# Performance work log

Measured on AMD Instinct MI355X. Metric: run time of the kernel, lower is better.

The kernel has to match this reference:

```python
import jax, jax.numpy as jnp
import numpy as np

B, L, C_S, H = 1, 512, 384, 12
D = C_S // H  # head_dim = 32


def setup_inputs() -> dict:
    key = jax.random.key(0)
    ks = jax.random.split(key, 12)
    sc = 1.0 / np.sqrt(C_S)
    inp = {
        "s": jax.random.normal(ks[0], (B, L, C_S), dtype=jnp.float32),
        "z": jax.random.normal(ks[1], (B, L, L, C_S), dtype=jnp.float32),
        "mask": jax.random.randint(ks[2], (B, L), 0, 2, dtype=jnp.int32),
        # learned params
        "Wq": jax.random.normal(ks[3], (C_S, H * D), dtype=jnp.float32) * sc,
        "bq": jnp.zeros((H * D,), dtype=jnp.float32),
        "Wkv": jax.random.normal(ks[4], (C_S, 2 * H * D), dtype=jnp.float32) * sc,
        "bkv": jnp.zeros((2 * H * D,), dtype=jnp.float32),
        "Wb": jax.random.normal(ks[5], (C_S, H), dtype=jnp.float32) * sc,
        "bb": jnp.zeros((H,), dtype=jnp.float32),
        "Wg": jax.random.normal(ks[6], (C_S, H), dtype=jnp.float32) * sc,
        "bg": jnp.zeros((H,), dtype=jnp.float32),
        "Wout": jax.random.normal(ks[7], (H * D, C_S), dtype=jnp.float32) * sc,
        "bout": jnp.zeros((C_S,), dtype=jnp.float32),
    }
    return inp


def reference(s, z, Wq, bq, Wkv, bkv, Wb, bb, Wg, bg, Wout, bout, mask):
    b, l, c = s.shape
    q = (s @ Wq + bq).reshape(b, l, H, D)                 # (B,L,h,d)
    kv = (s @ Wkv + bkv).reshape(b, l, 2, H, D)
    k, v = kv[:, :, 0], kv[:, :, 1]                       # (B,L,h,d)
    logits = jnp.einsum('blhd,bmhd->bhlm', q, k) * (D ** -0.5)
    bias = jnp.transpose(z @ Wb + bb, (0, 3, 1, 2))       # (B,h,L,L)
    logits = logits + bias
    gate = jax.nn.sigmoid(jnp.transpose(z @ Wg + bg, (0, 3, 1, 2)))
    maskf = mask.astype(logits.dtype)
    mask2d = maskf[:, :, None] * maskf[:, None, :]        # (B,L,L)
    logits = jnp.where(mask2d[:, None] < 0.5, jnp.asarray(-1e9, logits.dtype), logits)
    attn = jax.nn.softmax(logits, axis=-1) * gate         # (B,h,L,L)
    o = jnp.einsum('bhlm,bmhd->blhd', attn, v).reshape(b, l, H * D)
    return o @ Wout + bout
```

## Files before the change

kernel.cpp:

```cpp
#include <hip/hip_runtime.h>
#include <math.h>


__global__ __launch_bounds__(256) void sgemm_bias(const float* __restrict__ A, int lda,
                                                  const float* __restrict__ B, int ldb,
                                                  const float* __restrict__ bias,
                                                  float* __restrict__ C, int ldc, int K)
{
    __shared__ float As[32 * 36];
    __shared__ float Bs[32 * 68];

    const int t  = threadIdx.x;
    const int m0 = blockIdx.y * 32;
    const int n0 = blockIdx.x * 64;
    const int tx = t & 15;
    const int ty = t >> 4;

    float acc[2][4];
    #pragma unroll
    for (int i = 0; i < 2; ++i)
        #pragma unroll
        for (int j = 0; j < 4; ++j) acc[i][j] = 0.f;

    for (int kc = 0; kc < K; kc += 32) {
        __syncthreads();
        {
            int r = t >> 3, c = (t & 7) * 4;
            float4 av = *(const float4*)&A[(size_t)(m0 + r) * lda + kc + c];
            As[(c + 0) * 36 + r] = av.x;
            As[(c + 1) * 36 + r] = av.y;
            As[(c + 2) * 36 + r] = av.z;
            As[(c + 3) * 36 + r] = av.w;
        }
        #pragma unroll
        for (int i = 0; i < 2; ++i) {
            int slot = i * 256 + t;
            int r = slot >> 4, c = (slot & 15) * 4;
            *(float4*)&Bs[r * 68 + c] = *(const float4*)&B[(size_t)(kc + r) * ldb + n0 + c];
        }
        __syncthreads();
        #pragma unroll 8
        for (int k = 0; k < 32; ++k) {
            float2 a = *(const float2*)&As[k * 36 + ty * 2];
            float4 b = *(const float4*)&Bs[k * 68 + tx * 4];
            acc[0][0] = fmaf(a.x, b.x, acc[0][0]);
            acc[0][1] = fmaf(a.x, b.y, acc[0][1]);
            acc[0][2] = fmaf(a.x, b.z, acc[0][2]);
            acc[0][3] = fmaf(a.x, b.w, acc[0][3]);
            acc[1][0] = fmaf(a.y, b.x, acc[1][0]);
            acc[1][1] = fmaf(a.y, b.y, acc[1][1]);
            acc[1][2] = fmaf(a.y, b.z, acc[1][2]);
            acc[1][3] = fmaf(a.y, b.w, acc[1][3]);
        }
    }

    float4 bv = *(const float4*)&bias[n0 + tx * 4];
    #pragma unroll
    for (int im = 0; im < 2; ++im) {
        float4 r;
        r.x = acc[im][0] + bv.x;
        r.y = acc[im][1] + bv.y;
        r.z = acc[im][2] + bv.z;
        r.w = acc[im][3] + bv.w;
        *(float4*)&C[(size_t)(m0 + ty * 2 + im) * ldc + n0 + tx * 4] = r;
    }
}

__global__ __launch_bounds__(256) void wcat_kernel(const float* __restrict__ Wb,
                                                   const float* __restrict__ Wg,
                                                   float* __restrict__ wcat)
{
    for (int idx = threadIdx.x; idx < 24 * 384; idx += 256) {
        int hh = idx / 384, k = idx % 384;
        wcat[idx] = (hh < 12) ? Wb[k * 12 + hh] : Wg[k * 12 + (hh - 12)];
    }
}

__global__ __launch_bounds__(256) void biasgate_kernel(const float* __restrict__ z,
                                                       const float* __restrict__ wcat,
                                                       const float* __restrict__ bb,
                                                       const float* __restrict__ bg,
                                                       float* __restrict__ bias_out,
                                                       float* __restrict__ gate_out)
{
    const int t = threadIdx.x;
    const size_t p = (size_t)blockIdx.x * 256 + t;
    const float* zp = z + p * 384;

    float acc[24];
    #pragma unroll
    for (int h = 0; h < 24; ++h) acc[h] = 0.f;

    for (int c = 0; c < 12; ++c) {
        const int kc = c * 32;
        float4 zr[8];
        #pragma unroll
        for (int i = 0; i < 8; ++i)
            zr[i] = *(const float4*)&zp[kc + i * 4];
        #pragma unroll
        for (int k4 = 0; k4 < 8; ++k4) {
            const float4 zv = zr[k4];
            const float* wp = wcat + kc + k4 * 4;
            #pragma unroll
            for (int hh = 0; hh < 24; ++hh) {
                float4 w = *(const float4*)&wp[hh * 384];
                acc[hh] = fmaf(zv.x, w.x,
                          fmaf(zv.y, w.y,
                          fmaf(zv.z, w.z,
                          fmaf(zv.w, w.w, acc[hh]))));
            }
        }
    }

    #pragma unroll
    for (int hh = 0; hh < 12; ++hh)
        bias_out[(size_t)hh * 262144 + p] = acc[hh] + bb[hh];
    #pragma unroll
    for (int hh = 0; hh < 12; ++hh) {
        float x = acc[12 + hh] + bg[hh];
        gate_out[(size_t)hh * 262144 + p] = 1.f / (1.f + expf(-x));
    }
}

__global__ __launch_bounds__(256) void attn_kernel(const float* __restrict__ q_ws,
                                                   const float* __restrict__ kv_ws,
                                                   const float* __restrict__ bias_ws,
                                                   const float* __restrict__ gate_ws,
                                                   const int* __restrict__ mask,
                                                   float* __restrict__ o_ws)
{
    __shared__ float ql[16 * 36];
    __shared__ float kl[128 * 36];
    __shared__ float att[16 * 516];
    __shared__ int   mint[16];

    const int t  = threadIdx.x;
    const int h  = blockIdx.y;
    const int i0 = blockIdx.x * 16;

    for (int idx = t; idx < 512; idx += 256) {
        int ii = idx >> 5, d = idx & 31;
        ql[ii * 36 + d] = q_ws[(size_t)(i0 + ii) * 384 + h * 32 + d];
    }
    if (t < 16) mint[t] = mask[i0 + t];

    const float inv = 0.17677669529663687f;
    const int jl = t & 127;
    const int ip = t >> 7;

    for (int jc = 0; jc < 4; ++jc) {
        const int j0 = jc * 128;
        __syncthreads();
        for (int idx = t; idx < 4096; idx += 256) {
            int jj = idx >> 5, d = idx & 31;
            kl[jj * 36 + d] = kv_ws[(size_t)(j0 + jj) * 768 + h * 32 + d];
        }
        __syncthreads();
        float4 kr[8];
        #pragma unroll
        for (int x = 0; x < 8; ++x) kr[x] = *(const float4*)&kl[jl * 36 + x * 4];
        const int mj = mask[j0 + jl];
        #pragma unroll
        for (int rr = 0; rr < 8; ++rr) {
            int ii = ip + rr * 2;
            float dot = 0.f;
            #pragma unroll
            for (int x = 0; x < 8; ++x) {
                float4 qv = *(const float4*)&ql[ii * 36 + x * 4];
                dot = fmaf(kr[x].x, qv.x, dot);
                dot = fmaf(kr[x].y, qv.y, dot);
                dot = fmaf(kr[x].z, qv.z, dot);
                dot = fmaf(kr[x].w, qv.w, dot);
            }
            float bv = bias_ws[((size_t)h << 18) + (size_t)(i0 + ii) * 512 + j0 + jl];
            float lg = fmaf(dot, inv, bv);
            att[ii * 516 + j0 + jl] = (mint[ii] != 0 && mj != 0) ? lg : -1e9f;
        }
    }
    __syncthreads();

    {
        const int rr = t >> 4, g = t & 15;
        const int base = rr * 516 + g;
        float mx = -3.0e38f;
        #pragma unroll
        for (int n = 0; n < 32; ++n) mx = fmaxf(mx, att[base + n * 16]);
        #pragma unroll
        for (int off = 8; off >= 1; off >>= 1) mx = fmaxf(mx, __shfl_xor(mx, off));
        float sum = 0.f;
        #pragma unroll
        for (int n = 0; n < 32; ++n) {
            float e = expf(att[base + n * 16] - mx);
            att[base + n * 16] = e;
            sum += e;
        }
        #pragma unroll
        for (int off = 8; off >= 1; off >>= 1) sum += __shfl_xor(sum, off);
        float isum = 1.f / sum;
        const size_t gbase = ((size_t)h << 18) + (size_t)(i0 + rr) * 512 + g;
        #pragma unroll
        for (int n = 0; n < 32; ++n) {
            float gt = gate_ws[gbase + n * 16];
            att[base + n * 16] *= isum * gt;
        }
    }
    __syncthreads();

    {
        const int d = t & 31, grp = t >> 5;
        const float* vp = kv_ws + 384 + h * 32 + d;
        float a0 = 0.f, a1 = 0.f;
        #pragma unroll 8
        for (int j = 0; j < 512; ++j) {
            float vv = vp[(size_t)j * 768];
            a0 = fmaf(att[grp * 516 + j], vv, a0);
            a1 = fmaf(att[(grp + 8) * 516 + j], vv, a1);
        }
        o_ws[(size_t)(i0 + grp) * 384 + h * 32 + d]     = a0;
        o_ws[(size_t)(i0 + grp + 8) * 384 + h * 32 + d] = a1;
    }
}

extern "C" void kernel_launch(void* const* d_in, const int* in_sizes, int n_in,
                              void* d_out, int out_size, void* d_ws, size_t ws_size,
                              hipStream_t stream)
{
    const float* s    = (const float*)d_in[0];
    const float* z    = (const float*)d_in[1];
    const int*   mask = (const int*)  d_in[2];
    const float* Wq   = (const float*)d_in[3];
    const float* bq   = (const float*)d_in[4];
    const float* Wkv  = (const float*)d_in[5];
    const float* bkv  = (const float*)d_in[6];
    const float* Wb   = (const float*)d_in[7];
    const float* bb   = (const float*)d_in[8];
    const float* Wg   = (const float*)d_in[9];
    const float* bg   = (const float*)d_in[10];
    const float* Wout = (const float*)d_in[11];
    const float* bout = (const float*)d_in[12];
    float* out = (float*)d_out;

    float* ws      = (float*)d_ws;
    float* q_ws    = ws;
    float* kv_ws   = q_ws + 512 * 384;
    float* o_ws    = kv_ws + 512 * 768;
    float* bias_ws = o_ws + 512 * 384;
    float* gate_ws = bias_ws + 12 * 512 * 512;
    float* wcat_ws = gate_ws + 12 * 512 * 512;

    wcat_kernel<<<1, 256, 0, stream>>>(Wb, Wg, wcat_ws);
    sgemm_bias<<<dim3(384 / 64, 512 / 32), 256, 0, stream>>>(s, 384, Wq, 384, bq, q_ws, 384, 384);
    sgemm_bias<<<dim3(768 / 64, 512 / 32), 256, 0, stream>>>(s, 384, Wkv, 768, bkv, kv_ws, 768, 384);
    biasgate_kernel<<<1024, 256, 0, stream>>>(z, wcat_ws, bb, bg, bias_ws, gate_ws);
    attn_kernel<<<dim3(512 / 16, 12), 256, 0, stream>>>(q_ws, kv_ws, bias_ws, gate_ws, mask, o_ws);
    sgemm_bias<<<dim3(384 / 64, 512 / 32), 256, 0, stream>>>(o_ws, 384, Wout, 384, bout, out, 384, 384);
}
```

Before: 795.7 us.

## Split attention into softmax and PV kernels, prefetch z with nontemporal loads

The fused attention kernel becomes two kernels. The first computes masked logits and softmax per row in registers using warp shuffles, and writes the gated probabilities in place over the bias buffer. The second stages attention and V tiles in shared memory for the PV product. The z-projection kernel double-buffers its z loads with nontemporal loads and sets a min-blocks launch bound, and the weight-transpose kernel now runs on 36 blocks instead of one. The split adds a round trip of the attention matrix through global memory in exchange for more parallelism and simpler per-kernel structure.

```diff
diff --git a/kernel.cpp b/kernel.cpp
--- a/kernel.cpp
+++ b/kernel.cpp
@@ -1,6 +1,8 @@
 #include <hip/hip_runtime.h>
 #include <math.h>
 
+
+typedef float vf4 __attribute__((ext_vector_type(4)));
 
 __global__ __launch_bounds__(256) void sgemm_bias(const float* __restrict__ A, int lda,
                                                   const float* __restrict__ B, int ldb,
@@ -70,18 +72,19 @@
                                                    const float* __restrict__ Wg,
                                                    float* __restrict__ wcat)
 {
-    for (int idx = threadIdx.x; idx < 24 * 384; idx += 256) {
+    int idx = blockIdx.x * 256 + threadIdx.x;
+    if (idx < 24 * 384) {
         int hh = idx / 384, k = idx % 384;
         wcat[idx] = (hh < 12) ? Wb[k * 12 + hh] : Wg[k * 12 + (hh - 12)];
     }
 }
 
-__global__ __launch_bounds__(256) void biasgate_kernel(const float* __restrict__ z,
-                                                       const float* __restrict__ wcat,
-                                                       const float* __restrict__ bb,
-                                                       const float* __restrict__ bg,
-                                                       float* __restrict__ bias_out,
-                                                       float* __restrict__ gate_out)
+__global__ __launch_bounds__(256, 2) void biasgate_kernel(const float* __restrict__ z,
+                                                          const float* __restrict__ wcat,
+                                                          const float* __restrict__ bb,
+                                                          const float* __restrict__ bg,
+                                                          float* __restrict__ bias_out,
+                                                          float* __restrict__ gate_out)
 {
     const int t = threadIdx.x;
     const size_t p = (size_t)blockIdx.x * 256 + t;
@@ -91,15 +94,23 @@
     #pragma unroll
     for (int h = 0; h < 24; ++h) acc[h] = 0.f;
 
+    vf4 cur[8], nxt[8];
+    #pragma unroll
+    for (int i = 0; i < 8; ++i)
+        cur[i] = __builtin_nontemporal_load((const vf4*)&zp[i * 4]);
+
+    #pragma unroll 1
     for (int c = 0; c < 12; ++c) {
+        if (c < 11) {
+            const int kn = (c + 1) * 32;
+            #pragma unroll
+            for (int i = 0; i < 8; ++i)
+                nxt[i] = __builtin_nontemporal_load((const vf4*)&zp[kn + i * 4]);
+        }
         const int kc = c * 32;
-        float4 zr[8];
-        #pragma unroll
-        for (int i = 0; i < 8; ++i)
-            zr[i] = *(const float4*)&zp[kc + i * 4];
         #pragma unroll
         for (int k4 = 0; k4 < 8; ++k4) {
-            const float4 zv = zr[k4];
+            const vf4 zv = cur[k4];
             const float* wp = wcat + kc + k4 * 4;
             #pragma unroll
             for (int hh = 0; hh < 24; ++hh) {
@@ -110,6 +121,8 @@
                           fmaf(zv.w, w.w, acc[hh]))));
             }
         }
+        #pragma unroll
+        for (int i = 0; i < 8; ++i) cur[i] = nxt[i];
     }
 
     #pragma unroll
@@ -122,103 +135,119 @@
     }
 }
 
-__global__ __launch_bounds__(256) void attn_kernel(const float* __restrict__ q_ws,
-                                                   const float* __restrict__ kv_ws,
-                                                   const float* __restrict__ bias_ws,
-                                                   const float* __restrict__ gate_ws,
-                                                   const int* __restrict__ mask,
-                                                   float* __restrict__ o_ws)
-{
-    __shared__ float ql[16 * 36];
-    __shared__ float kl[128 * 36];
-    __shared__ float att[16 * 516];
-    __shared__ int   mint[16];
+__global__ __launch_bounds__(256) void attn_sm(const float* __restrict__ q_ws,
+                                               const float* __restrict__ kv_ws,
+                                               float* __restrict__ attn_ws,
+                                               const float* __restrict__ gate_ws,
+                                               const int* __restrict__ mask)
+{
+    __shared__ float ql[8 * 32];
+    __shared__ int   mi[8];
+
+    const int t  = threadIdx.x;
+    const int h  = blockIdx.y;
+    const int i0 = blockIdx.x * 8;
+    const int r  = t >> 5;
+    const int l  = t & 31;
+
+    ql[t] = q_ws[(size_t)(i0 + r) * 384 + h * 32 + l];
+    if (t < 8) mi[t] = mask[i0 + t];
+    __syncthreads();
+
+    const float inv = 0.17677669529663687f;
+    const size_t rowbase = ((size_t)h << 18) + (size_t)(i0 + r) * 512;
+    const int mrow = mi[r];
+
+    float lg[16];
+    float mx = -3.0e38f;
+    #pragma unroll
+    for (int m = 0; m < 16; ++m) {
+        const int j = m * 32 + l;
+        const float* kp = kv_ws + (size_t)j * 768 + h * 32;
+        float dot = 0.f;
+        #pragma unroll
+        for (int x = 0; x < 8; ++x) {
+            float4 kr = *(const float4*)&kp[x * 4];
+            float4 qv = *(const float4*)&ql[r * 32 + x * 4];
+            dot = fmaf(kr.x, qv.x, dot);
+            dot = fmaf(kr.y, qv.y, dot);
+            dot = fmaf(kr.z, qv.z, dot);
+            dot = fmaf(kr.w, qv.w, dot);
+        }
+        float bv = attn_ws[rowbase + j];
+        float lgv = fmaf(dot, inv, bv);
+        lg[m] = (mrow != 0 && mask[j] != 0) ? lgv : -1e9f;
+        mx = fmaxf(mx, lg[m]);
+    }
+    #pragma unroll
+    for (int off = 16; off >= 1; off >>= 1) mx = fmaxf(mx, __shfl_xor(mx, off, 32));
+
+    float sum = 0.f;
+    #pragma unroll
+    for (int m = 0; m < 16; ++m) {
+        lg[m] = expf(lg[m] - mx);
+        sum += lg[m];
+    }
+    #pragma unroll
+    for (int off = 16; off >= 1; off >>= 1) sum += __shfl_xor(sum, off, 32);
+    const float isum = 1.f / sum;
+
+    #pragma unroll
+    for (int m = 0; m < 16; ++m) {
+        const int j = m * 32 + l;
+        float gt = gate_ws[rowbase + j];
+        attn_ws[rowbase + j] = lg[m] * isum * gt;
+    }
+}
+
+__global__ __launch_bounds__(256) void attn_pv(const float* __restrict__ attn_ws,
+                                               const float* __restrict__ kv_ws,
+                                               float* __restrict__ o_ws)
+{
+    __shared__ float al[16 * 128];
+    __shared__ float vl[128 * 36];
 
     const int t  = threadIdx.x;
     const int h  = blockIdx.y;
     const int i0 = blockIdx.x * 16;
-
-    for (int idx = t; idx < 512; idx += 256) {
-        int ii = idx >> 5, d = idx & 31;
-        ql[ii * 36 + d] = q_ws[(size_t)(i0 + ii) * 384 + h * 32 + d];
-    }
-    if (t < 16) mint[t] = mask[i0 + t];
-
-    const float inv = 0.17677669529663687f;
-    const int jl = t & 127;
-    const int ip = t >> 7;
+    const int d  = t & 31;
+    const int ig = t >> 5;
+
+    float acc0 = 0.f, acc1 = 0.f;
 
     for (int jc = 0; jc < 4; ++jc) {
         const int j0 = jc * 128;
         __syncthreads();
-        for (int idx = t; idx < 4096; idx += 256) {
-            int jj = idx >> 5, d = idx & 31;
-            kl[jj * 36 + d] = kv_ws[(size_t)(j0 + jj) * 768 + h * 32 + d];
-        }
-        __syncthreads();
-        float4 kr[8];
-        #pragma unroll
-        for (int x = 0; x < 8; ++x) kr[x] = *(const float4*)&kl[jl * 36 + x * 4];
-        const int mj = mask[j0 + jl];
-        #pragma unroll
-        for (int rr = 0; rr < 8; ++rr) {
-            int ii = ip + rr * 2;
-            float dot = 0.f;
-            #pragma unroll
-            for (int x = 0; x < 8; ++x) {
-                float4 qv = *(const float4*)&ql[ii * 36 + x * 4];
-                dot = fmaf(kr[x].x, qv.x, dot);
-                dot = fmaf(kr[x].y, qv.y, dot);
-                dot = fmaf(kr[x].z, qv.z, dot);
-                dot = fmaf(kr[x].w, qv.w, dot);
-            }
-            float bv = bias_ws[((size_t)h << 18) + (size_t)(i0 + ii) * 512 + j0 + jl];
-            float lg = fmaf(dot, inv, bv);
-            att[ii * 516 + j0 + jl] = (mint[ii] != 0 && mj != 0) ? lg : -1e9f;
-        }
-    }
-    __syncthreads();
-
-    {
-        const int rr = t >> 4, g = t & 15;
-        const int base = rr * 516 + g;
-        float mx = -3.0e38f;
-        #pragma unroll
-        for (int n = 0; n < 32; ++n) mx = fmaxf(mx, att[base + n * 16]);
-        #pragma unroll
-        for (int off = 8; off >= 1; off >>= 1) mx = fmaxf(mx, __shfl_xor(mx, off));
-        float sum = 0.f;
-        #pragma unroll
-        for (int n = 0; n < 32; ++n) {
-            float e = expf(att[base + n * 16] - mx);
-            att[base + n * 16] = e;
-            sum += e;
-        }
-        #pragma unroll
-        for (int off = 8; off >= 1; off >>= 1) sum += __shfl_xor(sum, off);
-        float isum = 1.f / sum;
-        const size_t gbase = ((size_t)h << 18) + (size_t)(i0 + rr) * 512 + g;
-        #pragma unroll
-        for (int n = 0; n < 32; ++n) {
-            float gt = gate_ws[gbase + n * 16];
-            att[base + n * 16] *= isum * gt;
-        }
-    }
-    __syncthreads();
-
-    {
-        const int d = t & 31, grp = t >> 5;
-        const float* vp = kv_ws + 384 + h * 32 + d;
-        float a0 = 0.f, a1 = 0.f;
+        #pragma unroll
+        for (int i = 0; i < 2; ++i) {
+            int slot = i * 256 + t;
+            int row = slot >> 5, c4 = slot & 31;
+            *(float4*)&al[row * 128 + c4 * 4] =
+                *(const float4*)&attn_ws[((size_t)h << 18) + (size_t)(i0 + row) * 512 + j0 + c4 * 4];
+        }
+        #pragma unroll
+        for (int i = 0; i < 4; ++i) {
+            int slot = i * 256 + t;
+            int row = slot >> 3, c4 = slot & 7;
+            *(float4*)&vl[row * 36 + c4 * 4] =
+                *(const float4*)&kv_ws[(size_t)(j0 + row) * 768 + 384 + h * 32 + c4 * 4];
+        }
+        __syncthreads();
         #pragma unroll 8
-        for (int j = 0; j < 512; ++j) {
-            float vv = vp[(size_t)j * 768];
-            a0 = fmaf(att[grp * 516 + j], vv, a0);
-            a1 = fmaf(att[(grp + 8) * 516 + j], vv, a1);
-        }
-        o_ws[(size_t)(i0 + grp) * 384 + h * 32 + d]     = a0;
-        o_ws[(size_t)(i0 + grp + 8) * 384 + h * 32 + d] = a1;
-    }
+        for (int j4 = 0; j4 < 32; ++j4) {
+            float4 a0 = *(const float4*)&al[ig * 128 + j4 * 4];
+            float4 a1 = *(const float4*)&al[(ig + 8) * 128 + j4 * 4];
+            float v0 = vl[(j4 * 4 + 0) * 36 + d];
+            float v1 = vl[(j4 * 4 + 1) * 36 + d];
+            float v2 = vl[(j4 * 4 + 2) * 36 + d];
+            float v3 = vl[(j4 * 4 + 3) * 36 + d];
+            acc0 = fmaf(a0.x, v0, fmaf(a0.y, v1, fmaf(a0.z, v2, fmaf(a0.w, v3, acc0))));
+            acc1 = fmaf(a1.x, v0, fmaf(a1.y, v1, fmaf(a1.z, v2, fmaf(a1.w, v3, acc1))));
+        }
+    }
+
+    o_ws[(size_t)(i0 + ig) * 384 + h * 32 + d]     = acc0;
+    o_ws[(size_t)(i0 + ig + 8) * 384 + h * 32 + d] = acc1;
 }
 
 extern "C" void kernel_launch(void* const* d_in, const int* in_sizes, int n_in,
@@ -248,10 +277,11 @@
     float* gate_ws = bias_ws + 12 * 512 * 512;
     float* wcat_ws = gate_ws + 12 * 512 * 512;
 
-    wcat_kernel<<<1, 256, 0, stream>>>(Wb, Wg, wcat_ws);
+    wcat_kernel<<<36, 256, 0, stream>>>(Wb, Wg, wcat_ws);
     sgemm_bias<<<dim3(384 / 64, 512 / 32), 256, 0, stream>>>(s, 384, Wq, 384, bq, q_ws, 384, 384);
     sgemm_bias<<<dim3(768 / 64, 512 / 32), 256, 0, stream>>>(s, 384, Wkv, 768, bkv, kv_ws, 768, 384);
     biasgate_kernel<<<1024, 256, 0, stream>>>(z, wcat_ws, bb, bg, bias_ws, gate_ws);
-    attn_kernel<<<dim3(512 / 16, 12), 256, 0, stream>>>(q_ws, kv_ws, bias_ws, gate_ws, mask, o_ws);
+    attn_sm<<<dim3(512 / 8, 12), 256, 0, stream>>>(q_ws, kv_ws, bias_ws, gate_ws, mask);
+    attn_pv<<<dim3(512 / 16, 12), 256, 0, stream>>>(bias_ws, kv_ws, o_ws);
     sgemm_bias<<<dim3(384 / 64, 512 / 32), 256, 0, stream>>>(o_ws, 384, Wout, 384, bout, out, 384, 384);
 }
```

Result: slower. 813.4 us (+2.2%).

## Stage z tiles into LDS with async double-buffered global_load_lds in biasgate

Applied to the files above, without the earlier changes.

The bias/gate projection kernel now copies each 256-row by 32-column slice of z into shared memory using direct global-to-LDS loads. It double-buffers so the next slice is fetched while the current one is multiplied against the concatenated weights. The goal is better-coalesced streaming of the large z tensor and overlap of memory traffic with FMA work, instead of per-thread strided register loads. In exchange it uses 64KB of LDS per block, adds a barrier every iteration, and the per-thread LDS reads at a 32-float stride may cause bank conflicts. The weight transpose kernel is also spread across 36 blocks instead of one.

```diff
diff --git a/kernel.cpp b/kernel.cpp
--- a/kernel.cpp
+++ b/kernel.cpp
@@ -1,6 +1,10 @@
 #include <hip/hip_runtime.h>
 #include <math.h>
 
+
+typedef float vf4 __attribute__((ext_vector_type(4)));
+typedef __attribute__((address_space(3))) void       lds_vp;
+typedef __attribute__((address_space(1))) const void gm_vp;
 
 __global__ __launch_bounds__(256) void sgemm_bias(const float* __restrict__ A, int lda,
                                                   const float* __restrict__ B, int ldb,
@@ -70,7 +74,8 @@
                                                    const float* __restrict__ Wg,
                                                    float* __restrict__ wcat)
 {
-    for (int idx = threadIdx.x; idx < 24 * 384; idx += 256) {
+    int idx = blockIdx.x * 256 + threadIdx.x;
+    if (idx < 24 * 384) {
         int hh = idx / 384, k = idx % 384;
         wcat[idx] = (hh < 12) ? Wb[k * 12 + hh] : Wg[k * 12 + (hh - 12)];
     }
@@ -83,23 +88,47 @@
                                                        float* __restrict__ bias_out,
                                                        float* __restrict__ gate_out)
 {
-    const int t = threadIdx.x;
-    const size_t p = (size_t)blockIdx.x * 256 + t;
-    const float* zp = z + p * 384;
+    __shared__ float zt[2][256 * 32];
+
+    const int t  = threadIdx.x;
+    const size_t p0 = (size_t)blockIdx.x * 256;
+    const size_t p  = p0 + t;
+
+    const int wv   = t >> 6;
+    const int lane = t & 63;
+    const int lrow = lane >> 3;
+    const int lcol = (lane & 7) * 4;
 
     float acc[24];
     #pragma unroll
     for (int h = 0; h < 24; ++h) acc[h] = 0.f;
 
+    #pragma unroll
+    for (int i = 0; i < 8; ++i) {
+        const int row = wv * 64 + i * 8 + lrow;
+        __builtin_amdgcn_global_load_lds(
+            (gm_vp*)(z + (p0 + row) * 384 + lcol),
+            (lds_vp*)(&zt[0][row * 32 + lcol]), 16, 0, 0);
+    }
+    __syncthreads();
+
+    #pragma unroll 1
     for (int c = 0; c < 12; ++c) {
+        const int cur = c & 1;
+        if (c < 11) {
+            const int nk = (c + 1) * 32;
+            #pragma unroll
+            for (int i = 0; i < 8; ++i) {
+                const int row = wv * 64 + i * 8 + lrow;
+                __builtin_amdgcn_global_load_lds(
+                    (gm_vp*)(z + (p0 + row) * 384 + nk + lcol),
+                    (lds_vp*)(&zt[cur ^ 1][row * 32 + lcol]), 16, 0, 0);
+            }
+        }
         const int kc = c * 32;
-        float4 zr[8];
-        #pragma unroll
-        for (int i = 0; i < 8; ++i)
-            zr[i] = *(const float4*)&zp[kc + i * 4];
         #pragma unroll
         for (int k4 = 0; k4 < 8; ++k4) {
-            const float4 zv = zr[k4];
+            const vf4 zv = *(const vf4*)&zt[cur][t * 32 + k4 * 4];
             const float* wp = wcat + kc + k4 * 4;
             #pragma unroll
             for (int hh = 0; hh < 24; ++hh) {
@@ -110,6 +139,7 @@
                           fmaf(zv.w, w.w, acc[hh]))));
             }
         }
+        __syncthreads();
     }
 
     #pragma unroll
@@ -248,7 +278,7 @@
     float* gate_ws = bias_ws + 12 * 512 * 512;
     float* wcat_ws = gate_ws + 12 * 512 * 512;
 
-    wcat_kernel<<<1, 256, 0, stream>>>(Wb, Wg, wcat_ws);
+    wcat_kernel<<<36, 256, 0, stream>>>(Wb, Wg, wcat_ws);
     sgemm_bias<<<dim3(384 / 64, 512 / 32), 256, 0, stream>>>(s, 384, Wq, 384, bq, q_ws, 384, 384);
     sgemm_bias<<<dim3(768 / 64, 512 / 32), 256, 0, stream>>>(s, 384, Wkv, 768, bkv, kv_ws, 768, 384);
     biasgate_kernel<<<1024, 256, 0, stream>>>(z, wcat_ws, bb, bg, bias_ws, gate_ws);
```

Result: faster. 769.2 us (-3.3%).
